# Kernel optimization log

Hardware: AMD Instinct MI355X
Metric: run time of the kernel (lower is better)

## Reference

```python
import jax, jax.numpy as jnp
import numpy as np

N_VOXELS = 262144  # active output voxels (stride=1 -> same coord set as input)


def setup_inputs() -> dict:
    key = jax.random.key(0)
    k1, k2, k3, k4 = jax.random.split(key, 4)
    N, C_IN, C_OUT, K, M = N_VOXELS, 64, 64, 27, 65536
    x = jax.random.normal(k1, (N, C_IN), dtype=jnp.float32)
    W = jax.random.normal(k2, (K, C_IN, C_OUT), dtype=jnp.float32) * (1.0 / np.sqrt(C_IN * K))
    in_map = jax.random.randint(k3, (K, M), 0, N, dtype=jnp.int32)
    out_map = jax.random.randint(k4, (K, M), 0, N, dtype=jnp.int32)
    return {"x": x, "W": W, "in_map": in_map, "out_map": out_map}


def reference(x, W, in_map, out_map):
    # Sparse (Minkowski-style) convolution: gather -> per-offset GEMM -> scatter-add.
    # x: [N, Cin], W: [K, Cin, Cout], in_map/out_map: [K, M] indices into voxel list.
    N = x.shape[0]
    C_out = W.shape[-1]
    gathered = x[in_map]                              # [K, M, Cin]  (irregular gather)
    msg = jnp.einsum('kmc,kcd->kmd', gathered, W)     # [K, M, Cout] per-offset GEMM
    out = jnp.zeros((N, C_out), dtype=x.dtype)
    out = out.at[out_map.reshape(-1)].add(msg.reshape(-1, C_out))  # scatter-add
    return out
```

## Files before the change

kernel.cpp:

```cpp
#include <hip/hip_runtime.h>


typedef __attribute__((ext_vector_type(8))) short bf16x8;
typedef __attribute__((ext_vector_type(8))) unsigned short u16x8;
typedef __attribute__((ext_vector_type(4))) unsigned short u16x4;
typedef __attribute__((ext_vector_type(4))) float f32x4;
typedef __attribute__((ext_vector_type(2))) float f32x2;

constexpr int KOFF = 27;
constexpr int M = 65536;
constexpr int CIN = 64;
constexpr int COUT = 64;
constexpr int NVOX = 262144;
constexpr int NMSG = KOFF * M;
constexpr int TM_BLOCK = 512;
constexpr int TILES_PER_K = M / TM_BLOCK;
constexpr int SUBTILES = TM_BLOCK / (4 * 16);
constexpr int XCVT_BLOCKS = NVOX * CIN / 8 / 256;
constexpr int COUNT_BLOCKS = NMSG / 256;

static __device__ __forceinline__ short f2bf(float f) {
  unsigned u = __builtin_bit_cast(unsigned, f);
  unsigned r = (u + 0x7FFFu + ((u >> 16) & 1u)) >> 16;
  return (short)r;
}
static __device__ __forceinline__ float bf2f(unsigned short h) {
  return __builtin_bit_cast(float, (unsigned)h << 16);
}


__global__ __launch_bounds__(256) void prep_kernel(
    const float* __restrict__ x, const float* __restrict__ W,
    const int* __restrict__ out_map, unsigned short* __restrict__ xb,
    unsigned short* __restrict__ Wf, int* __restrict__ count, int xcvtBlocks) {
  const int b = blockIdx.x;
  if (b < xcvtBlocks) {
    int i = b * 256 + threadIdx.x;
    const float4* p = (const float4*)x + (size_t)i * 2;
    float4 a = p[0], q = p[1];
    u16x8 h;
    h[0] = (unsigned short)f2bf(a.x); h[1] = (unsigned short)f2bf(a.y);
    h[2] = (unsigned short)f2bf(a.z); h[3] = (unsigned short)f2bf(a.w);
    h[4] = (unsigned short)f2bf(q.x); h[5] = (unsigned short)f2bf(q.y);
    h[6] = (unsigned short)f2bf(q.z); h[7] = (unsigned short)f2bf(q.w);
    *(u16x8*)(xb + (size_t)i * 8) = h;
  } else if (b < xcvtBlocks + COUNT_BLOCKS) {
    int i = (b - xcvtBlocks) * 256 + threadIdx.x;
    atomicAdd(&count[out_map[i]], 1);
  } else {
    int k = b - xcvtBlocks - COUNT_BLOCKS;
    const float* Wk = W + (size_t)k * (CIN * COUT);
    unsigned short* dst = Wf + (size_t)k * 4096;
#pragma unroll
    for (int i = 0; i < 16; ++i) {
      int e = threadIdx.x * 16 + i;
      int j = e & 7, l = (e >> 3) & 63, tu = e >> 9;
      int t = tu >> 1, u = tu & 1;
      dst[e] = (unsigned short)f2bf(Wk[(u * 32 + (l >> 4) * 8 + j) * COUT + t * 16 + (l & 15)]);
    }
  }
}


__global__ __launch_bounds__(256) void scan1_kernel(const int* __restrict__ count,
                                                    int* __restrict__ cursor,
                                                    int* __restrict__ blockSums) {
  __shared__ int s[256];
  int t = threadIdx.x, i = blockIdx.x * 256 + t;
  int c = count[i];
  s[t] = c; __syncthreads();
  for (int off = 1; off < 256; off <<= 1) {
    int add = (t >= off) ? s[t - off] : 0;
    __syncthreads(); s[t] += add; __syncthreads();
  }
  cursor[i] = s[t] - c;
  if (t == 255) blockSums[blockIdx.x] = s[t];
}

__global__ __launch_bounds__(256) void scan2_kernel(int* __restrict__ bs) {
  __shared__ int s[256];
  int t = threadIdx.x;
  int v0 = bs[t*4], v1 = bs[t*4+1], v2 = bs[t*4+2], v3 = bs[t*4+3];
  int sum = v0 + v1 + v2 + v3;
  s[t] = sum; __syncthreads();
  for (int off = 1; off < 256; off <<= 1) {
    int add = (t >= off) ? s[t - off] : 0;
    __syncthreads(); s[t] += add; __syncthreads();
  }
  int run = s[t] - sum;
  bs[t*4] = run; run += v0;
  bs[t*4+1] = run; run += v1;
  bs[t*4+2] = run; run += v2;
  bs[t*4+3] = run;
}

__global__ __launch_bounds__(256) void scan3_kernel(int* __restrict__ cursor,
                                                    const int* __restrict__ blockBase) {
  int i = blockIdx.x * 256 + threadIdx.x;
  cursor[i] += blockBase[blockIdx.x];
}


template <bool BF16IN>
__global__ __launch_bounds__(256) void gemm_msg_kernel(
    const void* __restrict__ xin, const unsigned short* __restrict__ Wf,
    const int* __restrict__ in_map, const int* __restrict__ out_map,
    int* __restrict__ cursor, unsigned short* __restrict__ msg) {
  const int k = blockIdx.x / TILES_PER_K;
  const int mblock = (blockIdx.x % TILES_PER_K) * TM_BLOCK;
  const int wave = threadIdx.x >> 6;
  const int l = threadIdx.x & 63;
  const int lg = l >> 4;
  const int lr = l & 15;

  bf16x8 bfrag[4][2];
  const bf16x8* wf = (const bf16x8*)(Wf + (size_t)k * 4096);
#pragma unroll
  for (int t = 0; t < 4; ++t)
#pragma unroll
    for (int u = 0; u < 2; ++u)
      bfrag[t][u] = wf[(t * 2 + u) * 64 + l];

  const int mwave = mblock + wave * (TM_BLOCK / 4);
  const int rb = k * M + mwave;
  int slotA = atomicAdd(&cursor[out_map[rb + l]], 1);
  int slotB = atomicAdd(&cursor[out_map[rb + 64 + l]], 1);

  auto loadA = [&](int s, bf16x8& A0, bf16x8& A1) {
    int id = in_map[rb + s * 16 + lr];
    if (BF16IN) {
      const unsigned short* xr = (const unsigned short*)xin + (size_t)id * CIN + lg * 8;
      A0 = *(const bf16x8*)(xr);
      A1 = *(const bf16x8*)(xr + 32);
    } else {
      const float* xr = (const float*)xin + (size_t)id * CIN + lg * 8;
      float4 x0 = *(const float4*)(xr);
      float4 x1 = *(const float4*)(xr + 4);
      float4 x2 = *(const float4*)(xr + 32);
      float4 x3 = *(const float4*)(xr + 36);
      A0[0]=f2bf(x0.x); A0[1]=f2bf(x0.y); A0[2]=f2bf(x0.z); A0[3]=f2bf(x0.w);
      A0[4]=f2bf(x1.x); A0[5]=f2bf(x1.y); A0[6]=f2bf(x1.z); A0[7]=f2bf(x1.w);
      A1[0]=f2bf(x2.x); A1[1]=f2bf(x2.y); A1[2]=f2bf(x2.z); A1[3]=f2bf(x2.w);
      A1[4]=f2bf(x3.x); A1[5]=f2bf(x3.y); A1[6]=f2bf(x3.z); A1[7]=f2bf(x3.w);
    }
  };

  bf16x8 c0, c1, n0, n1;
  loadA(0, c0, c1);
  loadA(1, n0, n1);

#pragma unroll 1
  for (int s = 0; s < SUBTILES; ++s) {
    bf16x8 p0, p1;
    const bool have = (s + 2 < SUBTILES);
    if (have) loadA(s + 2, p0, p1);

    f32x4 acc[4] = {{0.f,0.f,0.f,0.f},{0.f,0.f,0.f,0.f},{0.f,0.f,0.f,0.f},{0.f,0.f,0.f,0.f}};
#pragma unroll
    for (int t = 0; t < 4; ++t) {
      acc[t] = __builtin_amdgcn_mfma_f32_16x16x32_bf16(c0, bfrag[t][0], acc[t], 0, 0, 0);
      acc[t] = __builtin_amdgcn_mfma_f32_16x16x32_bf16(c1, bfrag[t][1], acc[t], 0, 0, 0);
    }

    const int slotsrc = (s < 4) ? slotA : slotB;
#pragma unroll
    for (int r = 0; r < 4; ++r) {
      const int sl = __shfl(slotsrc, (s * 16 + lg * 4 + r) & 63, 64);
      u16x4 h;
      h[0] = (unsigned short)f2bf(acc[0][r]);
      h[1] = (unsigned short)f2bf(acc[1][r]);
      h[2] = (unsigned short)f2bf(acc[2][r]);
      h[3] = (unsigned short)f2bf(acc[3][r]);
      __builtin_nontemporal_store(h, (u16x4*)(msg + (size_t)sl * 64 + lr * 4));
    }

    c0 = n0; c1 = n1;
    if (have) { n0 = p0; n1 = p1; }
  }
}


__global__ __launch_bounds__(256) void gather_out_kernel(
    const unsigned short* __restrict__ msg, const int* __restrict__ cursorEnd,
    const int* __restrict__ count, float* __restrict__ out) {
  const int wid = (blockIdx.x * 256 + threadIdx.x) >> 6;
  const int p = threadIdx.x & 63;
  const int r = p >> 3;
  const int c = p & 7;
  const int o = wid * 8 + r;

  const int n = count[o];
  const int base = (n > 0) ? (cursorEnd[o] - n) : 0;
  const unsigned short* src = msg + (size_t)base * 64 + c * 8;

  u16x8 v[8];
#pragma unroll
  for (int i = 0; i < 8; ++i) {
    int safe = (i < n) ? i : 0;
    v[i] = __builtin_nontemporal_load((const u16x8*)(src + (size_t)safe * 64));
  }
  float acc[8] = {};
#pragma unroll
  for (int i = 0; i < 8; ++i) {
    float m = (i < n) ? 1.0f : 0.0f;
#pragma unroll
    for (int d = 0; d < 8; ++d)
      acc[d] = fmaf(m, bf2f((unsigned short)v[i][d]), acc[d]);
  }
  for (int i = 8; i < n; ++i) {
    u16x8 t = __builtin_nontemporal_load((const u16x8*)(src + (size_t)i * 64));
#pragma unroll
    for (int d = 0; d < 8; ++d) acc[d] += bf2f((unsigned short)t[d]);
  }

  float* orow = out + (size_t)o * 64 + 2 * c;
  f32x2 s0 = {acc[0], acc[4]};
  f32x2 s1 = {acc[1], acc[5]};
  f32x2 s2 = {acc[2], acc[6]};
  f32x2 s3 = {acc[3], acc[7]};
  __builtin_nontemporal_store(s0, (f32x2*)(orow));
  __builtin_nontemporal_store(s1, (f32x2*)(orow + 16));
  __builtin_nontemporal_store(s2, (f32x2*)(orow + 32));
  __builtin_nontemporal_store(s3, (f32x2*)(orow + 48));
}


__global__ __launch_bounds__(256) void spconv_atomic_kernel(
    const float* __restrict__ x, const float* __restrict__ W,
    const int* __restrict__ in_map, const int* __restrict__ out_map,
    float* __restrict__ out) {
  const int k = blockIdx.x / TILES_PER_K;
  const int mblock = (blockIdx.x % TILES_PER_K) * TM_BLOCK;
  const int wave = threadIdx.x >> 6;
  const int l = threadIdx.x & 63;
  const int lg = l >> 4;
  const int lr = l & 15;
  bf16x8 bfrag[4][2];
  const float* Wk = W + (size_t)k * (CIN * COUT);
#pragma unroll
  for (int t = 0; t < 4; ++t)
#pragma unroll
    for (int u = 0; u < 2; ++u)
#pragma unroll
      for (int j = 0; j < 8; ++j)
        bfrag[t][u][j] = f2bf(Wk[(u * 32 + lg * 8 + j) * COUT + t * 16 + lr]);
  const int mwave = mblock + wave * (TM_BLOCK / 4);
#pragma unroll 1
  for (int s = 0; s < SUBTILES; ++s) {
    const int mbase = mwave + s * 16;
    const int in_idx = in_map[k * M + mbase + lr];
    const float* xr = x + (size_t)in_idx * CIN + lg * 8;
    float4 x0 = *(const float4*)(xr);
    float4 x1 = *(const float4*)(xr + 4);
    float4 x2 = *(const float4*)(xr + 32);
    float4 x3 = *(const float4*)(xr + 36);
    bf16x8 a0, a1;
    a0[0]=f2bf(x0.x); a0[1]=f2bf(x0.y); a0[2]=f2bf(x0.z); a0[3]=f2bf(x0.w);
    a0[4]=f2bf(x1.x); a0[5]=f2bf(x1.y); a0[6]=f2bf(x1.z); a0[7]=f2bf(x1.w);
    a1[0]=f2bf(x2.x); a1[1]=f2bf(x2.y); a1[2]=f2bf(x2.z); a1[3]=f2bf(x2.w);
    a1[4]=f2bf(x3.x); a1[5]=f2bf(x3.y); a1[6]=f2bf(x3.z); a1[7]=f2bf(x3.w);
    f32x4 acc[4] = {{0.f,0.f,0.f,0.f},{0.f,0.f,0.f,0.f},{0.f,0.f,0.f,0.f},{0.f,0.f,0.f,0.f}};
#pragma unroll
    for (int t = 0; t < 4; ++t) {
      acc[t] = __builtin_amdgcn_mfma_f32_16x16x32_bf16(a0, bfrag[t][0], acc[t], 0, 0, 0);
      acc[t] = __builtin_amdgcn_mfma_f32_16x16x32_bf16(a1, bfrag[t][1], acc[t], 0, 0, 0);
    }
    const int obase = k * M + mbase + lg * 4;
    int oidx[4];
#pragma unroll
    for (int r = 0; r < 4; ++r) oidx[r] = out_map[obase + r];
#pragma unroll
    for (int t = 0; t < 4; ++t)
#pragma unroll
      for (int r = 0; r < 4; ++r)
        atomicAdd(out + (size_t)oidx[r] * COUT + t * 16 + lr, acc[t][r]);
  }
}

extern "C" void kernel_launch(void* const* d_in, const int* in_sizes, int n_in,
                              void* d_out, int out_size, void* d_ws, size_t ws_size,
                              hipStream_t stream) {
  const float* x = (const float*)d_in[0];
  const float* W = (const float*)d_in[1];
  const int* in_map = (const int*)d_in[2];
  const int* out_map = (const int*)d_in[3];
  float* out = (float*)d_out;
  char* ws = (char*)d_ws;

  const size_t msg_b = (size_t)NMSG * 128;
  const size_t xb_b = (size_t)NVOX * CIN * 2;
  const size_t wf_b = (size_t)KOFF * 4096 * 2;
  const size_t cnt_b = (size_t)NVOX * 4;
  auto pad = [](size_t b) { return (b + 255) & ~(size_t)255; };

  size_t need_p1 = pad(msg_b) + pad(wf_b) + 2 * pad(cnt_b) + pad(1024 * 4);
  size_t need_p0 = need_p1 + pad(xb_b);
  bool useXb = (ws_size >= need_p0);

  if (ws_size < need_p1) {
    hipMemsetAsync(d_out, 0, (size_t)out_size * sizeof(float), stream);
    spconv_atomic_kernel<<<dim3(KOFF * TILES_PER_K), dim3(256), 0, stream>>>(
        x, W, in_map, out_map, out);
    return;
  }

  size_t off = 0;
  unsigned short* msg = (unsigned short*)(ws + off); off += pad(msg_b);
  unsigned short* xb = nullptr;
  if (useXb) { xb = (unsigned short*)(ws + off); off += pad(xb_b); }
  unsigned short* Wf = (unsigned short*)(ws + off); off += pad(wf_b);
  int* count  = (int*)(ws + off); off += pad(cnt_b);
  int* cursor = (int*)(ws + off); off += pad(cnt_b);
  int* bsum   = (int*)(ws + off);

  hipMemsetAsync(count, 0, cnt_b, stream);

  int xcvtBlocks = useXb ? XCVT_BLOCKS : 0;
  prep_kernel<<<dim3(xcvtBlocks + COUNT_BLOCKS + KOFF), dim3(256), 0, stream>>>(
      x, W, out_map, xb, Wf, count, xcvtBlocks);

  scan1_kernel<<<dim3(NVOX / 256), dim3(256), 0, stream>>>(count, cursor, bsum);
  scan2_kernel<<<dim3(1), dim3(256), 0, stream>>>(bsum);
  scan3_kernel<<<dim3(NVOX / 256), dim3(256), 0, stream>>>(cursor, bsum);

  if (useXb)
    gemm_msg_kernel<true><<<dim3(KOFF * TILES_PER_K), dim3(256), 0, stream>>>(
        (const void*)xb, Wf, in_map, out_map, cursor, msg);
  else
    gemm_msg_kernel<false><<<dim3(KOFF * TILES_PER_K), dim3(256), 0, stream>>>(
        (const void*)x, Wf, in_map, out_map, cursor, msg);

  gather_out_kernel<<<dim3(NVOX / 32), dim3(256), 0, stream>>>(msg, cursor, count, out);
}
```

Baseline: 257.1 us.

## Move slot atomics out of GEMM into separate scatter kernel producing permutation

```diff
diff --git a/kernel.cpp b/kernel.cpp
--- a/kernel.cpp
+++ b/kernel.cpp
@@ -32,7 +32,7 @@
 __global__ __launch_bounds__(256) void prep_kernel(
     const float* __restrict__ x, const float* __restrict__ W,
     const int* __restrict__ out_map, unsigned short* __restrict__ xb,
-    unsigned short* __restrict__ Wf, int* __restrict__ count, int xcvtBlocks) {
+    unsigned short* __restrict__ Wf, int* __restrict__ cursor, int xcvtBlocks) {
   const int b = blockIdx.x;
   if (b < xcvtBlocks) {
     int i = b * 256 + threadIdx.x;
@@ -46,7 +46,7 @@
     *(u16x8*)(xb + (size_t)i * 8) = h;
   } else if (b < xcvtBlocks + COUNT_BLOCKS) {
     int i = (b - xcvtBlocks) * 256 + threadIdx.x;
-    atomicAdd(&count[out_map[i]], 1);
+    atomicAdd(&cursor[out_map[i]], 1);
   } else {
     int k = b - xcvtBlocks - COUNT_BLOCKS;
     const float* Wk = W + (size_t)k * (CIN * COUT);
@@ -62,12 +62,11 @@
 }
 
 
-__global__ __launch_bounds__(256) void scan1_kernel(const int* __restrict__ count,
-                                                    int* __restrict__ cursor,
+__global__ __launch_bounds__(256) void scan1_kernel(int* __restrict__ cursor,
                                                     int* __restrict__ blockSums) {
   __shared__ int s[256];
   int t = threadIdx.x, i = blockIdx.x * 256 + t;
-  int c = count[i];
+  int c = cursor[i];
   s[t] = c; __syncthreads();
   for (int off = 1; off < 256; off <<= 1) {
     int add = (t >= off) ? s[t - off] : 0;
@@ -101,11 +100,19 @@
 }
 
 
+__global__ __launch_bounds__(256) void scatter_kernel(const int* __restrict__ out_map,
+                                                      int* __restrict__ cursor,
+                                                      int* __restrict__ perm) {
+  int i = blockIdx.x * 256 + threadIdx.x;
+  perm[i] = atomicAdd(&cursor[out_map[i]], 1);
+}
+
+
 template <bool BF16IN>
 __global__ __launch_bounds__(256) void gemm_msg_kernel(
     const void* __restrict__ xin, const unsigned short* __restrict__ Wf,
-    const int* __restrict__ in_map, const int* __restrict__ out_map,
-    int* __restrict__ cursor, unsigned short* __restrict__ msg) {
+    const int* __restrict__ in_map, const int* __restrict__ perm,
+    unsigned short* __restrict__ msg) {
   const int k = blockIdx.x / TILES_PER_K;
   const int mblock = (blockIdx.x % TILES_PER_K) * TM_BLOCK;
   const int wave = threadIdx.x >> 6;
@@ -123,8 +130,6 @@
 
   const int mwave = mblock + wave * (TM_BLOCK / 4);
   const int rb = k * M + mwave;
-  int slotA = atomicAdd(&cursor[out_map[rb + l]], 1);
-  int slotB = atomicAdd(&cursor[out_map[rb + 64 + l]], 1);
 
   auto loadA = [&](int s, bf16x8& A0, bf16x8& A1) {
     int id = in_map[rb + s * 16 + lr];
@@ -162,10 +167,10 @@
       acc[t] = __builtin_amdgcn_mfma_f32_16x16x32_bf16(c1, bfrag[t][1], acc[t], 0, 0, 0);
     }
 
-    const int slotsrc = (s < 4) ? slotA : slotB;
+    const int* pr = perm + rb + s * 16 + lg * 4;
 #pragma unroll
     for (int r = 0; r < 4; ++r) {
-      const int sl = __shfl(slotsrc, (s * 16 + lg * 4 + r) & 63, 64);
+      const int sl = pr[r];
       u16x4 h;
       h[0] = (unsigned short)f2bf(acc[0][r]);
       h[1] = (unsigned short)f2bf(acc[1][r]);
@@ -182,15 +187,16 @@
 
 __global__ __launch_bounds__(256) void gather_out_kernel(
     const unsigned short* __restrict__ msg, const int* __restrict__ cursorEnd,
-    const int* __restrict__ count, float* __restrict__ out) {
+    float* __restrict__ out) {
   const int wid = (blockIdx.x * 256 + threadIdx.x) >> 6;
   const int p = threadIdx.x & 63;
   const int r = p >> 3;
   const int c = p & 7;
   const int o = wid * 8 + r;
 
-  const int n = count[o];
-  const int base = (n > 0) ? (cursorEnd[o] - n) : 0;
+  const int end = cursorEnd[o];
+  const int base = (o > 0) ? cursorEnd[o - 1] : 0;
+  const int n = end - base;
   const unsigned short* src = msg + (size_t)base * 64 + c * 8;
 
   u16x8 v[8];
@@ -287,13 +293,15 @@
   float* out = (float*)d_out;
   char* ws = (char*)d_ws;
 
-  const size_t msg_b = (size_t)NMSG * 128;
-  const size_t xb_b = (size_t)NVOX * CIN * 2;
-  const size_t wf_b = (size_t)KOFF * 4096 * 2;
-  const size_t cnt_b = (size_t)NVOX * 4;
+  const size_t msg_b  = (size_t)NMSG * 128;
+  const size_t xb_b   = (size_t)NVOX * CIN * 2;
+  const size_t perm_b = (size_t)NMSG * 4;
+  const size_t wf_b   = (size_t)KOFF * 4096 * 2;
+  const size_t cur_b  = (size_t)NVOX * 4;
+  const size_t bs_b   = 1024 * 4;
   auto pad = [](size_t b) { return (b + 255) & ~(size_t)255; };
 
-  size_t need_p1 = pad(msg_b) + pad(wf_b) + 2 * pad(cnt_b) + pad(1024 * 4);
+  size_t need_p1 = pad(msg_b) + pad(perm_b) + pad(wf_b) + pad(cur_b) + pad(bs_b);
   size_t need_p0 = need_p1 + pad(xb_b);
   bool useXb = (ws_size >= need_p0);
 
@@ -308,27 +316,28 @@
   unsigned short* msg = (unsigned short*)(ws + off); off += pad(msg_b);
   unsigned short* xb = nullptr;
   if (useXb) { xb = (unsigned short*)(ws + off); off += pad(xb_b); }
+  int* perm = (int*)(ws + off); off += pad(perm_b);
   unsigned short* Wf = (unsigned short*)(ws + off); off += pad(wf_b);
-  int* count  = (int*)(ws + off); off += pad(cnt_b);
-  int* cursor = (int*)(ws + off); off += pad(cnt_b);
+  int* cursor = (int*)(ws + off); off += pad(cur_b);
   int* bsum   = (int*)(ws + off);
 
-  hipMemsetAsync(count, 0, cnt_b, stream);
+  hipMemsetAsync(cursor, 0, cur_b, stream);
 
   int xcvtBlocks = useXb ? XCVT_BLOCKS : 0;
   prep_kernel<<<dim3(xcvtBlocks + COUNT_BLOCKS + KOFF), dim3(256), 0, stream>>>(
-      x, W, out_map, xb, Wf, count, xcvtBlocks);
-
-  scan1_kernel<<<dim3(NVOX / 256), dim3(256), 0, stream>>>(count, cursor, bsum);
+      x, W, out_map, xb, Wf, cursor, xcvtBlocks);
+
+  scan1_kernel<<<dim3(NVOX / 256), dim3(256), 0, stream>>>(cursor, bsum);
   scan2_kernel<<<dim3(1), dim3(256), 0, stream>>>(bsum);
   scan3_kernel<<<dim3(NVOX / 256), dim3(256), 0, stream>>>(cursor, bsum);
+  scatter_kernel<<<dim3(NMSG / 256), dim3(256), 0, stream>>>(out_map, cursor, perm);
 
   if (useXb)
     gemm_msg_kernel<true><<<dim3(KOFF * TILES_PER_K), dim3(256), 0, stream>>>(
-        (const void*)xb, Wf, in_map, out_map, cursor, msg);
+        (const void*)xb, Wf, in_map, perm, msg);
   else
     gemm_msg_kernel<false><<<dim3(KOFF * TILES_PER_K), dim3(256), 0, stream>>>(
-        (const void*)x, Wf, in_map, out_map, cursor, msg);
-
-  gather_out_kernel<<<dim3(NVOX / 32), dim3(256), 0, stream>>>(msg, cursor, count, out);
-}
+        (const void*)x, Wf, in_map, perm, msg);
+
+  gather_out_kernel<<<dim3(NVOX / 32), dim3(256), 0, stream>>>(msg, cursor, out);
+}
```

New measurement: 289.0 us. 12.4% more time.
